# Kernel tuning notes

Hardware: AMD Instinct MI355X
Metric: run time of the kernel (lower is better)

Reference implementation:

```python
import jax, jax.numpy as jnp
import numpy as np
from jax import lax

# 8-bit symmetric quantization: clip bound = 2**(prec-1) - 1
CLIP = 127.0
EPS = 1e-6  # epsilon in scale denominator to avoid div-by-zero (mirrors QuantOps bound epsilon)


def setup_inputs() -> dict:
    key = jax.random.key(0)
    k1, k2 = jax.random.split(key)
    B, CIN, COUT = 8192, 4096, 8192
    act = jax.random.normal(k1, (B, CIN), dtype=jnp.float32)
    w = jax.random.normal(k2, (CIN, COUT), dtype=jnp.float32)
    return {"act": act, "w": w}


def reference(act, w):
    # --- activation quantization: per-input-channel symmetric scale, shape (1, Cin) ---
    act_bound = jnp.max(jnp.abs(act), axis=0, keepdims=True) + EPS     # (1, Cin)
    act_scale = CLIP / act_bound                                        # (1, Cin)
    act_q = jnp.clip(jnp.round(act * act_scale), -CLIP, CLIP)           # int values in fp32

    # fold inverse activation scale into weight rows: w_scaled_rows = (1/act_scale) * w
    w_scaled = w * (1.0 / act_scale).reshape(-1, 1)                     # (Cin, Cout)

    # --- weight quantization: per-output-channel symmetric scale, shape (1, Cout) ---
    w_bound = jnp.max(jnp.abs(w_scaled), axis=0, keepdims=True) + EPS   # (1, Cout)
    w_scale = CLIP / w_bound                                            # (1, Cout)
    w_q = jnp.clip(jnp.round(w_scaled * w_scale), -CLIP, CLIP)

    out_i32 = lax.dot_general(
        act_q.astype(jnp.int8),
        w_q.astype(jnp.int8),
        dimension_numbers=(((1,), (0,)), ((), ())),
        preferred_element_type=jnp.int32,
    )
    out = out_i32.astype(jnp.float32)

    # inline dequant by per-output-channel weight scale (act scale already folded into w)
    return (out * (1.0 / w_scale)).astype(jnp.float32)
```

## Files before the change

kernel.cpp:

```cpp
#include <hip/hip_runtime.h>
#include <hip/hip_bf16.h>
#include <stdint.h>

#define BDIM 8192
#define CIN  4096
#define COUT 8192
#define EPSQ 1e-6f

typedef int v4i __attribute__((ext_vector_type(4)));

#define GLD16_TO_LDS(gp, lp)                                                   \
    __builtin_amdgcn_global_load_lds(                                          \
        (const __attribute__((address_space(1))) void*)(gp),                   \
        (__attribute__((address_space(3))) void*)(lp), 16, 0, 0)

__device__ __forceinline__ int q8i(float x) {
    float r = rintf(x);
    r = fminf(127.0f, fmaxf(-127.0f, r));
    return (int)r;
}

__global__ void act_absmax_kernel(const float* __restrict__ act,
                                  int* __restrict__ amax_bits) {
    int c4 = (blockIdx.x << 8) + threadIdx.x;
    int r0 = blockIdx.y << 6;
    const float4* p = (const float4*)act + (size_t)r0 * (CIN / 4) + c4;
    float mx = 0.f, my = 0.f, mz = 0.f, mw = 0.f;
#pragma unroll 4
    for (int r = 0; r < 64; ++r) {
        float4 v = p[(size_t)r * (CIN / 4)];
        mx = fmaxf(mx, fabsf(v.x));
        my = fmaxf(my, fabsf(v.y));
        mz = fmaxf(mz, fabsf(v.z));
        mw = fmaxf(mw, fabsf(v.w));
    }
    int c = c4 << 2;
    atomicMax(amax_bits + c + 0, __float_as_int(mx));
    atomicMax(amax_bits + c + 1, __float_as_int(my));
    atomicMax(amax_bits + c + 2, __float_as_int(mz));
    atomicMax(amax_bits + c + 3, __float_as_int(mw));
}

__global__ void act_quant_kernel(const float4* __restrict__ act4,
                                 const int4* __restrict__ amax_bits4,
                                 float* __restrict__ inv_as,
                                 int* __restrict__ actq_packed) {
    int flat4 = blockIdx.x * 256 + threadIdx.x;
    int c4 = flat4 & ((CIN / 4) - 1);
    float4 v = act4[flat4];
    int4 mb = amax_bits4[c4];
    float sx = 127.0f / (__int_as_float(mb.x) + EPSQ);
    float sy = 127.0f / (__int_as_float(mb.y) + EPSQ);
    float sz = 127.0f / (__int_as_float(mb.z) + EPSQ);
    float sw = 127.0f / (__int_as_float(mb.w) + EPSQ);
    int q0 = q8i(v.x * sx), q1 = q8i(v.y * sy), q2 = q8i(v.z * sz), q3 = q8i(v.w * sw);
    int packed = (q0 & 0xff) | ((q1 & 0xff) << 8) | ((q2 & 0xff) << 16) | ((q3 & 0xff) << 24);
    actq_packed[flat4] = packed;
    if (flat4 < CIN / 4) {
        int c = c4 << 2;
        inv_as[c + 0] = 1.0f / sx;
        inv_as[c + 1] = 1.0f / sy;
        inv_as[c + 2] = 1.0f / sz;
        inv_as[c + 3] = 1.0f / sw;
    }
}

__global__ void w_absmax_kernel(const float* __restrict__ w,
                                const float* __restrict__ inv_as,
                                int* __restrict__ wmax_bits) {
    int c4 = (blockIdx.x << 8) + threadIdx.x;
    int k0 = blockIdx.y << 5;
    const float4* p = (const float4*)w + (size_t)k0 * (COUT / 4) + c4;
    float mx = 0.f, my = 0.f, mz = 0.f, mw = 0.f;
#pragma unroll 4
    for (int r = 0; r < 32; ++r) {
        float ia = inv_as[k0 + r];
        float4 v = p[(size_t)r * (COUT / 4)];
        mx = fmaxf(mx, fabsf(v.x * ia));
        my = fmaxf(my, fabsf(v.y * ia));
        mz = fmaxf(mz, fabsf(v.z * ia));
        mw = fmaxf(mw, fabsf(v.w * ia));
    }
    int c = c4 << 2;
    atomicMax(wmax_bits + c + 0, __float_as_int(mx));
    atomicMax(wmax_bits + c + 1, __float_as_int(my));
    atomicMax(wmax_bits + c + 2, __float_as_int(mz));
    atomicMax(wmax_bits + c + 3, __float_as_int(mw));
}

__global__ void w_quant_t_kernel(const float* __restrict__ w,
                                 const float* __restrict__ inv_as,
                                 const int* __restrict__ wmax_bits,
                                 signed char* __restrict__ wqT) {
    __shared__ int tile32[16][65];
    int t = threadIdx.x;
    int k0 = blockIdx.x << 6;
    int j0 = blockIdx.y << 6;
    int tx = t & 63;
    int ty = t >> 6;
    int j = j0 + tx;
    float wscale = 127.0f / (__int_as_float(wmax_bits[j]) + EPSQ);
#pragma unroll
    for (int r = 0; r < 4; ++r) {
        int a = r * 4 + ty;
        int kb = k0 + (a << 2);
        int packed = 0;
#pragma unroll
        for (int u = 0; u < 4; ++u) {
            int k = kb + u;
            float wsc = w[(size_t)k * COUT + j] * inv_as[k];
            int q = q8i(wsc * wscale);
            packed |= (q & 0xff) << (8 * u);
        }
        tile32[a][tx] = packed;
    }
    __syncthreads();
    int j_loc = t >> 2;
    int c = t & 3;
    int4 v;
    v.x = tile32[c * 4 + 0][j_loc];
    v.y = tile32[c * 4 + 1][j_loc];
    v.z = tile32[c * 4 + 2][j_loc];
    v.w = tile32[c * 4 + 3][j_loc];
    *(int4*)(wqT + (size_t)(j0 + j_loc) * CIN + k0 + c * 16) = v;
}

__global__ __launch_bounds__(512, 2) void gemm_i8_kernel(
    const signed char* __restrict__ Aq,
    const signed char* __restrict__ Bq,
    const int* __restrict__ wmax_bits,
    float* __restrict__ out) {
    __shared__ __align__(16) signed char lds[131072];
    signed char* As = lds;
    signed char* Bs = lds + 65536;

    const int tid = threadIdx.x;
    const int wave = tid >> 6;
    const int lane = tid & 63;
    const int g = lane >> 4;
    const int l16 = lane & 15;

    const int bid = blockIdx.x;
    const int swz = (bid & 7) * 128 + (bid >> 3);
    const int bm = (swz >> 5) << 8;
    const int bn = (swz & 31) << 8;

    const int wm128 = (wave >> 2) << 7;
    const int wn64 = (wave & 3) << 6;

    const int m = tid & 255;
    const int gq = tid >> 8;
    const signed char* aP = Aq + ((size_t)(bm + m) << 12) + (gq << 4);
    const signed char* bP = Bq + ((size_t)(bn + m) << 12) + (gq << 4);
    const int ldsOff = tid << 4;

    const int offA = ((g << 8) + wm128 + l16) << 4;
    const int offB = ((g << 8) + wn64 + l16) << 4;

    v4i acc[8][4] = {};

#define STAGE_STEP(t_)                                                         \
    do {                                                                       \
        signed char* As_ = As + (((t_) & 3) << 14);                            \
        signed char* Bs_ = Bs + (((t_) & 3) << 14);                            \
        const int kb_ = (t_) << 6;                                             \
        GLD16_TO_LDS(aP + kb_,      As_ + ldsOff);                             \
        GLD16_TO_LDS(aP + kb_ + 32, As_ + 8192 + ldsOff);                      \
        GLD16_TO_LDS(bP + kb_,      Bs_ + ldsOff);                             \
        GLD16_TO_LDS(bP + kb_ + 32, Bs_ + 8192 + ldsOff);                      \
    } while (0)

#define COMPUTE_STEP(s_)                                                       \
    do {                                                                       \
        const signed char* Ab_ = As + (((s_) & 3) << 14);                      \
        const signed char* Bb_ = Bs + (((s_) & 3) << 14);                      \
        v4i af_[8], bf_[4];                                                    \
        _Pragma("unroll")                                                      \
        for (int t = 0; t < 8; ++t)                                            \
            af_[t] = *(const v4i*)(Ab_ + offA + (t << 8));                     \
        _Pragma("unroll")                                                      \
        for (int t = 0; t < 4; ++t)                                            \
            bf_[t] = *(const v4i*)(Bb_ + offB + (t << 8));                     \
        __builtin_amdgcn_s_setprio(1);                                         \
        _Pragma("unroll")                                                      \
        for (int tm = 0; tm < 8; ++tm)                                         \
            _Pragma("unroll")                                                  \
            for (int tn = 0; tn < 4; ++tn)                                     \
                acc[tm][tn] = __builtin_amdgcn_mfma_i32_16x16x64_i8(           \
                    af_[tm], bf_[tn], acc[tm][tn], 0, 0, 0);                   \
        __builtin_amdgcn_s_setprio(0);                                         \
    } while (0)

    STAGE_STEP(0);
    STAGE_STEP(1);
    STAGE_STEP(2);
    asm volatile("s_waitcnt vmcnt(8)" ::: "memory");

#pragma unroll 1
    for (int s = 0; s < 61; ++s) {
        __builtin_amdgcn_s_barrier();
        __builtin_amdgcn_sched_barrier(0);
        STAGE_STEP(s + 3);
        COMPUTE_STEP(s);
        asm volatile("s_waitcnt vmcnt(8)" ::: "memory");
        __builtin_amdgcn_sched_barrier(0);
    }
    __builtin_amdgcn_s_barrier();
    __builtin_amdgcn_sched_barrier(0);
    COMPUTE_STEP(61);
    asm volatile("s_waitcnt vmcnt(4)" ::: "memory");
    __builtin_amdgcn_sched_barrier(0);
    __builtin_amdgcn_s_barrier();
    __builtin_amdgcn_sched_barrier(0);
    COMPUTE_STEP(62);
    asm volatile("s_waitcnt vmcnt(0)" ::: "memory");
    __builtin_amdgcn_sched_barrier(0);
    __builtin_amdgcn_s_barrier();
    __builtin_amdgcn_sched_barrier(0);
    COMPUTE_STEP(63);

#undef STAGE_STEP
#undef COMPUTE_STEP

#pragma unroll
    for (int tn = 0; tn < 4; ++tn) {
        int col = bn + wn64 + (tn << 4) + l16;
        float wscale = 127.0f / (__int_as_float(wmax_bits[col]) + EPSQ);
        float invws = 1.0f / wscale;
#pragma unroll
        for (int tm = 0; tm < 8; ++tm) {
            int row0 = bm + wm128 + (tm << 4) + (g << 2);
#pragma unroll
            for (int r = 0; r < 4; ++r)
                out[((size_t)(row0 + r) << 13) + col] = (float)acc[tm][tn][r] * invws;
        }
    }
}

extern "C" void kernel_launch(void* const* d_in, const int* in_sizes, int n_in,
                              void* d_out, int out_size, void* d_ws, size_t ws_size,
                              hipStream_t stream) {
    const float* act = (const float*)d_in[0];
    const float* w   = (const float*)d_in[1];
    float* out = (float*)d_out;
    char* ws = (char*)d_ws;

    int*   amax_bits = (int*)ws;
    float* inv_as    = (float*)(ws + 16384);
    int*   wmax_bits = (int*)(ws + 32768);
    signed char* actq = (signed char*)(ws + 65536);
    signed char* wqT  = (signed char*)(ws + 65536 + (size_t)BDIM * CIN);

    act_absmax_kernel<<<dim3(4, 128), 256, 0, stream>>>(act, amax_bits);
    act_quant_kernel<<<(BDIM * CIN / 4) / 256, 256, 0, stream>>>(
        (const float4*)act, (const int4*)amax_bits, inv_as, (int*)actq);
    w_absmax_kernel<<<dim3(8, 128), 256, 0, stream>>>(w, inv_as, wmax_bits);
    w_quant_t_kernel<<<dim3(64, 128), 256, 0, stream>>>(w, inv_as, wmax_bits, wqT);
    gemm_i8_kernel<<<COUT / 256 * (BDIM / 256), 512, 0, stream>>>(
        actq, wqT, wmax_bits, out);
}
```

Measured before the change: 924.2 us.

## Split GEMM main loop into half-steps, retile weight quant, and remap blocks per XCD

```diff
diff --git a/kernel.cpp b/kernel.cpp
--- a/kernel.cpp
+++ b/kernel.cpp
@@ -23,11 +23,11 @@
 __global__ void act_absmax_kernel(const float* __restrict__ act,
                                   int* __restrict__ amax_bits) {
     int c4 = (blockIdx.x << 8) + threadIdx.x;
-    int r0 = blockIdx.y << 6;
+    int r0 = blockIdx.y << 5;
     const float4* p = (const float4*)act + (size_t)r0 * (CIN / 4) + c4;
     float mx = 0.f, my = 0.f, mz = 0.f, mw = 0.f;
 #pragma unroll 4
-    for (int r = 0; r < 64; ++r) {
+    for (int r = 0; r < 32; ++r) {
         float4 v = p[(size_t)r * (CIN / 4)];
         mx = fmaxf(mx, fabsf(v.x));
         my = fmaxf(my, fabsf(v.y));
@@ -69,11 +69,11 @@
                                 const float* __restrict__ inv_as,
                                 int* __restrict__ wmax_bits) {
     int c4 = (blockIdx.x << 8) + threadIdx.x;
-    int k0 = blockIdx.y << 5;
+    int k0 = blockIdx.y << 4;
     const float4* p = (const float4*)w + (size_t)k0 * (COUT / 4) + c4;
     float mx = 0.f, my = 0.f, mz = 0.f, mw = 0.f;
 #pragma unroll 4
-    for (int r = 0; r < 32; ++r) {
+    for (int r = 0; r < 16; ++r) {
         float ia = inv_as[k0 + r];
         float4 v = p[(size_t)r * (COUT / 4)];
         mx = fmaxf(mx, fabsf(v.x * ia));
@@ -92,37 +92,41 @@
                                  const float* __restrict__ inv_as,
                                  const int* __restrict__ wmax_bits,
                                  signed char* __restrict__ wqT) {
-    __shared__ int tile32[16][65];
+    __shared__ float lf[32 * 132];
     int t = threadIdx.x;
-    int k0 = blockIdx.x << 6;
-    int j0 = blockIdx.y << 6;
-    int tx = t & 63;
-    int ty = t >> 6;
-    int j = j0 + tx;
-    float wscale = 127.0f / (__int_as_float(wmax_bits[j]) + EPSQ);
-#pragma unroll
-    for (int r = 0; r < 4; ++r) {
-        int a = r * 4 + ty;
-        int kb = k0 + (a << 2);
-        int packed = 0;
-#pragma unroll
-        for (int u = 0; u < 4; ++u) {
-            int k = kb + u;
-            float wsc = w[(size_t)k * COUT + j] * inv_as[k];
-            int q = q8i(wsc * wscale);
-            packed |= (q & 0xff) << (8 * u);
-        }
-        tile32[a][tx] = packed;
+    int k0 = blockIdx.x << 7;
+    int j0 = blockIdx.y << 5;
+    const float4* w4 = (const float4*)w;
+#pragma unroll
+    for (int it = 0; it < 4; ++it) {
+        int idx = it * 256 + t;
+        int kk = idx >> 3;
+        int j4 = idx & 7;
+        float4 v = w4[(size_t)(k0 + kk) * (COUT / 4) + (j0 >> 2) + j4];
+        lf[(j4 * 4 + 0) * 132 + kk] = v.x;
+        lf[(j4 * 4 + 1) * 132 + kk] = v.y;
+        lf[(j4 * 4 + 2) * 132 + kk] = v.z;
+        lf[(j4 * 4 + 3) * 132 + kk] = v.w;
     }
     __syncthreads();
-    int j_loc = t >> 2;
-    int c = t & 3;
-    int4 v;
-    v.x = tile32[c * 4 + 0][j_loc];
-    v.y = tile32[c * 4 + 1][j_loc];
-    v.z = tile32[c * 4 + 2][j_loc];
-    v.w = tile32[c * 4 + 3][j_loc];
-    *(int4*)(wqT + (size_t)(j0 + j_loc) * CIN + k0 + c * 16) = v;
+#pragma unroll
+    for (int it = 0; it < 4; ++it) {
+        int kq = t & 31;
+        int jl = (t >> 5) + (it << 3);
+        int j = j0 + jl;
+        float wscale = 127.0f / (__int_as_float(wmax_bits[j]) + EPSQ);
+        float4 f = *(const float4*)(lf + jl * 132 + (kq << 2));
+        int kb = k0 + (kq << 2);
+        float w0 = f.x * inv_as[kb + 0];
+        float w1 = f.y * inv_as[kb + 1];
+        float w2 = f.z * inv_as[kb + 2];
+        float w3 = f.w * inv_as[kb + 3];
+        int q0 = q8i(w0 * wscale), q1 = q8i(w1 * wscale);
+        int q2 = q8i(w2 * wscale), q3 = q8i(w3 * wscale);
+        int packed = (q0 & 0xff) | ((q1 & 0xff) << 8) |
+                     ((q2 & 0xff) << 16) | ((q3 & 0xff) << 24);
+        *(int*)(wqT + (size_t)j * CIN + kb) = packed;
+    }
 }
 
 __global__ __launch_bounds__(512, 2) void gemm_i8_kernel(
@@ -141,9 +145,10 @@
     const int l16 = lane & 15;
 
     const int bid = blockIdx.x;
-    const int swz = (bid & 7) * 128 + (bid >> 3);
-    const int bm = (swz >> 5) << 8;
-    const int bn = (swz & 31) << 8;
+    const int xcd = bid & 7, idx = bid >> 3;
+    const int rg = xcd >> 2, cg = xcd & 3;
+    const int bm = (((rg << 4) + (idx >> 3)) << 8);
+    const int bn = (((cg << 3) + (idx & 7)) << 8);
 
     const int wm128 = (wave >> 2) << 7;
     const int wn64 = (wave & 3) << 6;
@@ -158,69 +163,114 @@
     const int offB = ((g << 8) + wn64 + l16) << 4;
 
     v4i acc[8][4] = {};
-
-#define STAGE_STEP(t_)                                                         \
-    do {                                                                       \
-        signed char* As_ = As + (((t_) & 3) << 14);                            \
-        signed char* Bs_ = Bs + (((t_) & 3) << 14);                            \
+    v4i fA0[4], fA1[4], fB[4];
+
+#define STAGE_A(t_)                                                            \
+    do {                                                                       \
+        signed char* d_ = As + (((t_) & 3) << 14);                             \
         const int kb_ = (t_) << 6;                                             \
-        GLD16_TO_LDS(aP + kb_,      As_ + ldsOff);                             \
-        GLD16_TO_LDS(aP + kb_ + 32, As_ + 8192 + ldsOff);                      \
-        GLD16_TO_LDS(bP + kb_,      Bs_ + ldsOff);                             \
-        GLD16_TO_LDS(bP + kb_ + 32, Bs_ + 8192 + ldsOff);                      \
-    } while (0)
-
-#define COMPUTE_STEP(s_)                                                       \
+        GLD16_TO_LDS(aP + kb_,      d_ + ldsOff);                              \
+        GLD16_TO_LDS(aP + kb_ + 32, d_ + 8192 + ldsOff);                       \
+    } while (0)
+#define STAGE_B(t_)                                                            \
+    do {                                                                       \
+        signed char* d_ = Bs + (((t_) & 3) << 14);                             \
+        const int kb_ = (t_) << 6;                                             \
+        GLD16_TO_LDS(bP + kb_,      d_ + ldsOff);                              \
+        GLD16_TO_LDS(bP + kb_ + 32, d_ + 8192 + ldsOff);                       \
+    } while (0)
+#define READ_FA0(s_)                                                           \
     do {                                                                       \
         const signed char* Ab_ = As + (((s_) & 3) << 14);                      \
+        _Pragma("unroll")                                                      \
+        for (int t = 0; t < 4; ++t)                                            \
+            fA0[t] = *(const v4i*)(Ab_ + offA + (t << 8));                     \
+    } while (0)
+#define READ_FA1(s_)                                                           \
+    do {                                                                       \
+        const signed char* Ab_ = As + (((s_) & 3) << 14);                      \
+        _Pragma("unroll")                                                      \
+        for (int t = 0; t < 4; ++t)                                            \
+            fA1[t] = *(const v4i*)(Ab_ + offA + ((t + 4) << 8));               \
+    } while (0)
+#define READ_FB(s_)                                                            \
+    do {                                                                       \
         const signed char* Bb_ = Bs + (((s_) & 3) << 14);                      \
-        v4i af_[8], bf_[4];                                                    \
-        _Pragma("unroll")                                                      \
-        for (int t = 0; t < 8; ++t)                                            \
-            af_[t] = *(const v4i*)(Ab_ + offA + (t << 8));                     \
         _Pragma("unroll")                                                      \
         for (int t = 0; t < 4; ++t)                                            \
-            bf_[t] = *(const v4i*)(Bb_ + offB + (t << 8));                     \
+            fB[t] = *(const v4i*)(Bb_ + offB + (t << 8));                      \
+    } while (0)
+#define MFMA_LO                                                                \
+    do {                                                                       \
         __builtin_amdgcn_s_setprio(1);                                         \
         _Pragma("unroll")                                                      \
-        for (int tm = 0; tm < 8; ++tm)                                         \
+        for (int tm = 0; tm < 4; ++tm)                                         \
             _Pragma("unroll")                                                  \
             for (int tn = 0; tn < 4; ++tn)                                     \
                 acc[tm][tn] = __builtin_amdgcn_mfma_i32_16x16x64_i8(           \
-                    af_[tm], bf_[tn], acc[tm][tn], 0, 0, 0);                   \
+                    fA0[tm], fB[tn], acc[tm][tn], 0, 0, 0);                    \
         __builtin_amdgcn_s_setprio(0);                                         \
     } while (0)
-
-    STAGE_STEP(0);
-    STAGE_STEP(1);
-    STAGE_STEP(2);
+#define MFMA_HI                                                                \
+    do {                                                                       \
+        __builtin_amdgcn_s_setprio(1);                                         \
+        _Pragma("unroll")                                                      \
+        for (int tm = 0; tm < 4; ++tm)                                         \
+            _Pragma("unroll")                                                  \
+            for (int tn = 0; tn < 4; ++tn)                                     \
+                acc[tm + 4][tn] = __builtin_amdgcn_mfma_i32_16x16x64_i8(       \
+                    fA1[tm], fB[tn], acc[tm + 4][tn], 0, 0, 0);                \
+        __builtin_amdgcn_s_setprio(0);                                         \
+    } while (0)
+
+    STAGE_A(0); STAGE_B(0);
+    STAGE_A(1); STAGE_B(1);
+    STAGE_A(2); STAGE_B(2);
     asm volatile("s_waitcnt vmcnt(8)" ::: "memory");
+    __builtin_amdgcn_s_barrier();
+    READ_FA0(0);
+    READ_FB(0);
 
 #pragma unroll 1
     for (int s = 0; s < 61; ++s) {
         __builtin_amdgcn_s_barrier();
         __builtin_amdgcn_sched_barrier(0);
-        STAGE_STEP(s + 3);
-        COMPUTE_STEP(s);
-        asm volatile("s_waitcnt vmcnt(8)" ::: "memory");
+        STAGE_A(s + 3);
+        MFMA_LO;
+        READ_FA1(s);
+        asm volatile("s_waitcnt vmcnt(6)" ::: "memory");
         __builtin_amdgcn_sched_barrier(0);
-    }
+        __builtin_amdgcn_s_barrier();
+        __builtin_amdgcn_sched_barrier(0);
+        STAGE_B(s + 3);
+        MFMA_HI;
+        READ_FA0(s + 1);
+        READ_FB(s + 1);
+        __builtin_amdgcn_sched_barrier(0);
+    }
+
+    asm volatile("s_waitcnt vmcnt(0)" ::: "memory");
     __builtin_amdgcn_s_barrier();
     __builtin_amdgcn_sched_barrier(0);
-    COMPUTE_STEP(61);
-    asm volatile("s_waitcnt vmcnt(4)" ::: "memory");
-    __builtin_amdgcn_sched_barrier(0);
-    __builtin_amdgcn_s_barrier();
-    __builtin_amdgcn_sched_barrier(0);
-    COMPUTE_STEP(62);
-    asm volatile("s_waitcnt vmcnt(0)" ::: "memory");
-    __builtin_amdgcn_sched_barrier(0);
-    __builtin_amdgcn_s_barrier();
-    __builtin_amdgcn_sched_barrier(0);
-    COMPUTE_STEP(63);
-
-#undef STAGE_STEP
-#undef COMPUTE_STEP
+    MFMA_LO;
+    READ_FA1(61);
+    MFMA_HI;
+    READ_FA0(62); READ_FB(62);
+    MFMA_LO;
+    READ_FA1(62);
+    MFMA_HI;
+    READ_FA0(63); READ_FB(63);
+    MFMA_LO;
+    READ_FA1(63);
+    MFMA_HI;
+
+#undef STAGE_A
+#undef STAGE_B
+#undef READ_FA0
+#undef READ_FA1
+#undef READ_FB
+#undef MFMA_LO
+#undef MFMA_HI
 
 #pragma unroll
     for (int tn = 0; tn < 4; ++tn) {
@@ -251,11 +301,11 @@
     signed char* actq = (signed char*)(ws + 65536);
     signed char* wqT  = (signed char*)(ws + 65536 + (size_t)BDIM * CIN);
 
-    act_absmax_kernel<<<dim3(4, 128), 256, 0, stream>>>(act, amax_bits);
+    act_absmax_kernel<<<dim3(4, 256), 256, 0, stream>>>(act, amax_bits);
     act_quant_kernel<<<(BDIM * CIN / 4) / 256, 256, 0, stream>>>(
         (const float4*)act, (const int4*)amax_bits, inv_as, (int*)actq);
-    w_absmax_kernel<<<dim3(8, 128), 256, 0, stream>>>(w, inv_as, wmax_bits);
-    w_quant_t_kernel<<<dim3(64, 128), 256, 0, stream>>>(w, inv_as, wmax_bits, wqT);
+    w_absmax_kernel<<<dim3(8, 256), 256, 0, stream>>>(w, inv_as, wmax_bits);
+    w_quant_t_kernel<<<dim3(32, 256), 256, 0, stream>>>(w, inv_as, wmax_bits, wqT);
     gemm_i8_kernel<<<COUT / 256 * (BDIM / 256), 512, 0, stream>>>(
         actq, wqT, wmax_bits, out);
 }
```

Result: faster. 875.1 us (-5.3%).
